# Performance work log

Measured on AMD Instinct MI355X. Metric: run time of the kernel, lower is better.

## Reference

```python
import jax, jax.numpy as jnp
import numpy as np

C = 64          # channels
K = 15          # sum(shell_sizes)=1+14
H = 32          # neighbors per query
N = 50000       # support points (== query points M)
RADIUS = 1.0
SIGMA = 0.7
INF = 1e6
BN_EPS = 1e-5


def _init_kernel_points(key):
    # stand-in for load_kernels: 1 center point + 14 points on a sphere shell
    pts = jax.random.normal(key, (K - 1, 3), dtype=jnp.float32)
    pts = pts / jnp.linalg.norm(pts, axis=1, keepdims=True) * RADIUS
    return jnp.concatenate([jnp.zeros((1, 3), jnp.float32), pts], axis=0)


def setup_inputs() -> dict:
    key = jax.random.key(0)
    ks = jax.random.split(key, 10)
    q_pts = jax.random.normal(ks[0], (N, 3), dtype=jnp.float32)
    s_pts = jax.random.normal(ks[1], (N, 3), dtype=jnp.float32)
    s_feats = jax.random.normal(ks[2], (N, C), dtype=jnp.float32)
    neighb_inds = jax.random.randint(ks[3], (N, H), 0, N)
    kernel_points = _init_kernel_points(ks[4])
    # alpha_mlp: Linear(C->C, no bias) -> BatchNorm -> LeakyReLU(0.1) -> Linear(C->K*C)
    lim1 = 1.0 / np.sqrt(C)
    W1 = jax.random.uniform(ks[5], (C, C), jnp.float32, -lim1, lim1)
    gamma = jnp.ones((C,), jnp.float32)
    beta = jnp.zeros((C,), jnp.float32)
    W2 = jax.random.uniform(ks[6], (C, K * C), jnp.float32, -lim1, lim1)
    b2 = jax.random.uniform(ks[7], (K * C,), jnp.float32, -lim1, lim1)
    return {"q_pts": q_pts, "s_pts": s_pts, "s_feats": s_feats,
            "neighb_inds": neighb_inds, "kernel_points": kernel_points,
            "W1": W1, "gamma": gamma, "beta": beta, "W2": W2, "b2": b2}


def reference(q_pts, s_pts, s_feats, neighb_inds, kernel_points, W1, gamma, beta, W2, b2):
    M = q_pts.shape[0]
    # alpha_mlp on pooled (= center) features: (M, C) -> (M, K*C)
    h = s_feats @ W1
    mu = jnp.mean(h, axis=0)
    var = jnp.var(h, axis=0)
    h = (h - mu) / jnp.sqrt(var + BN_EPS) * gamma + beta
    h = jax.nn.leaky_relu(h, 0.1)
    conv_weights = (h @ W2 + b2).reshape(M, K, C)

    # gather neighbor features with a zero padding row (index N -> zeros)
    padded_feats = jnp.concatenate([s_feats, jnp.zeros((1, C), s_feats.dtype)], axis=0)
    neighbor_feats = padded_feats[neighb_inds]                 # (M, H, C)

    # relative neighbor positions with inf padding point
    s_pts_pad = jnp.concatenate([s_pts, jnp.full((1, 3), INF, s_pts.dtype)], axis=0)
    neighbors = s_pts_pad[neighb_inds] - q_pts[:, None, :]     # (M, H, 3)

    # kernel-point influence: nearest kernel point + linear influence
    diff = neighbors[:, :, None, :] - kernel_points            # (M, H, K, 3)
    sq_d = jnp.sum(diff * diff, axis=-1)                       # (M, H, K)
    nn_sq = jnp.min(sq_d, axis=-1)                             # (M, H)
    nn_idx = jnp.argmin(sq_d, axis=-1)                         # (M, H)
    infl = jnp.clip(1.0 - jnp.sqrt(nn_sq) / SIGMA, 0.0)        # (M, H)

    # per-neighbor channel weights from the MLP output, gathered by 1nn kernel point
    nw = jnp.take_along_axis(conv_weights, nn_idx[:, :, None], axis=1)  # (M, H, C)
    nw = nw * infl[:, :, None]

    # weighted aggregation (merge=mul, aggr=sum over neighbors)
    return jnp.sum(neighbor_feats * nw, axis=1)                # (M, C)
```

## Files before the change

### kernel.cpp

```cpp
#include <hip/hip_runtime.h>
#include <math.h>

#define N_PTS 50000
#define CCH   64
#define KP    15
#define NH    32
#define SIGMA 0.7f
#define BN_EPS 1e-5f
#define LEAKY 0.1f
#define QB    16
#define CWS   18
#define STATS_BLOCKS 1024

typedef short bf16x8 __attribute__((ext_vector_type(8)));
typedef float floatx4 __attribute__((ext_vector_type(4)));

__device__ __forceinline__ unsigned short f2b(float f) {
    union { float f; unsigned u; } v; v.f = f;
    return (unsigned short)((v.u + 0x7FFFu + ((v.u >> 16) & 1u)) >> 16);
}
__device__ __forceinline__ float b2f(unsigned short b) {
    union { unsigned u; float f; } v; v.u = ((unsigned)b) << 16;
    return v.f;
}

__global__ __launch_bounds__(256) void k_prep(const float* __restrict__ sf,
                                              const float* __restrict__ W1,
                                              const float* __restrict__ W2,
                                              float* __restrict__ bn,
                                              unsigned short* __restrict__ hst,
                                              unsigned short* __restrict__ w2b,
                                              unsigned short* __restrict__ sfb) {
    int t = threadIdx.x;
    if (blockIdx.x >= STATS_BLOCKS) {
        int g = (blockIdx.x - STATS_BLOCKS) * 256 + t;
        int lane = g & 63, s = (g >> 6) & 1, tt = g >> 7;
        int col = lane & 15, quad = lane >> 4;
        int base = (s * 32 + quad * 8) * 960 + tt * 16 + col;
        ushort4 lo, hi;
        lo.x = f2b(W2[base + 0 * 960]); lo.y = f2b(W2[base + 1 * 960]);
        lo.z = f2b(W2[base + 2 * 960]); lo.w = f2b(W2[base + 3 * 960]);
        hi.x = f2b(W2[base + 4 * 960]); hi.y = f2b(W2[base + 5 * 960]);
        hi.z = f2b(W2[base + 6 * 960]); hi.w = f2b(W2[base + 7 * 960]);
        *(ushort4*)(w2b + g * 8)     = lo;
        *(ushort4*)(w2b + g * 8 + 4) = hi;
        return;
    }
    int c = t & 63, ml = t >> 6;
    float w1c[64];
    #pragma unroll
    for (int i = 0; i < 64; ++i) w1c[i] = W1[i * 64 + c];
    __shared__ float rows[4][64];
    float acc_s = 0.f, acc_q = 0.f;
    for (int m0 = blockIdx.x * 4; m0 < N_PTS; m0 += STATS_BLOCKS * 4) {
        __syncthreads();
        float v = sf[m0 * 64 + t];
        ((float*)rows)[t] = v;
        sfb[m0 * 64 + t] = f2b(v);
        __syncthreads();
        float h = 0.f;
        #pragma unroll
        for (int i4 = 0; i4 < 16; ++i4) {
            float4 r = *(const float4*)&rows[ml][i4 * 4];
            h += r.x * w1c[i4 * 4] + r.y * w1c[i4 * 4 + 1]
               + r.z * w1c[i4 * 4 + 2] + r.w * w1c[i4 * 4 + 3];
        }
        acc_s += h;
        acc_q += h * h;
        hst[(m0 + ml) * 64 + c] = f2b(h);
    }
    __shared__ float red[2][256];
    red[0][t] = acc_s; red[1][t] = acc_q;
    __syncthreads();
    if (t < 64) {
        float s = red[0][t] + red[0][64 + t] + red[0][128 + t] + red[0][192 + t];
        float q = red[1][t] + red[1][64 + t] + red[1][128 + t] + red[1][192 + t];
        atomicAdd(&bn[t], s);
        atomicAdd(&bn[64 + t], q);
    }
}

__global__ __launch_bounds__(256, 4) void k_main(
    const float* __restrict__ q_pts, const float* __restrict__ s_pts,
    const unsigned short* __restrict__ sfb, const int* __restrict__ nb,
    const float* __restrict__ kpts, const float* __restrict__ gamma,
    const float* __restrict__ beta, const float* __restrict__ bn,
    const float* __restrict__ b2, const unsigned short* __restrict__ w2b,
    const unsigned short* __restrict__ hst, float* __restrict__ out) {

    __shared__ __align__(16) unsigned short cwT[960 * CWS];
    __shared__ float abS[128];
    __shared__ int      nCnt[QB];
    __shared__ unsigned nPack[QB][NH];
    __shared__ float    nInf[QB][NH];

    int t = threadIdx.x;
    int lane = t & 63, wv = t >> 6;
    int m0 = blockIdx.x * QB;

    if (t < 64) {
        float mu  = bn[t] * (1.0f / N_PTS);
        float var = bn[64 + t] * (1.0f / N_PTS) - mu * mu;
        float a   = gamma[t] * rsqrtf(var + BN_EPS);
        abS[t]      = a;
        abS[64 + t] = beta[t] - mu * a;
    } else if (t >= 64 && t < 64 + QB) {
        nCnt[t - 64] = 0;
    }
    ((unsigned*)nPack)[t]    = 0u;
    ((unsigned*)nPack)[t + 256] = 0u;
    ((float*)nInf)[t]        = 0.f;
    ((float*)nInf)[t + 256]  = 0.f;
    __syncthreads();

    int row = lane & 15, half = lane >> 4;
    bf16x8 a0, a1;
    {
        const unsigned short* hrow = hst + (m0 + row) * 64 + half * 8;
        bf16x8 r0 = *(const bf16x8*)(hrow);
        bf16x8 r1 = *(const bf16x8*)(hrow + 32);
        #pragma unroll
        for (int j = 0; j < 8; ++j) {
            int c0 = half * 8 + j;
            float g0 = abS[c0] * b2f((unsigned short)r0[j]) + abS[64 + c0];
            g0 = g0 > 0.f ? g0 : LEAKY * g0;
            a0[j] = (short)f2b(g0);
            int c1 = 32 + c0;
            float g1 = abS[c1] * b2f((unsigned short)r1[j]) + abS[64 + c1];
            g1 = g1 > 0.f ? g1 : LEAKY * g1;
            a1[j] = (short)f2b(g1);
        }
    }

    {
        int col = lane & 15, quad = lane >> 4;
        for (int ti = 0; ti < 15; ++ti) {
            int tt = wv * 15 + ti;
            bf16x8 bf0 = *(const bf16x8*)(w2b + ((tt * 2 + 0) * 64 + lane) * 8);
            bf16x8 bf1 = *(const bf16x8*)(w2b + ((tt * 2 + 1) * 64 + lane) * 8);
            floatx4 acc = {0.f, 0.f, 0.f, 0.f};
            acc = __builtin_amdgcn_mfma_f32_16x16x32_bf16(a0, bf0, acc, 0, 0, 0);
            acc = __builtin_amdgcn_mfma_f32_16x16x32_bf16(a1, bf1, acc, 0, 0, 0);
            int n = tt * 16 + col;
            float bb = b2[n];
            unsigned short* dst = &cwT[n * CWS + quad * 4];
            ushort2 w01, w23;
            w01.x = f2b(acc[0] + bb); w01.y = f2b(acc[1] + bb);
            w23.x = f2b(acc[2] + bb); w23.y = f2b(acc[3] + bb);
            *(ushort2*)(dst)     = w01;
            *(ushort2*)(dst + 2) = w23;
        }
    }

    float kpr[45];
    #pragma unroll
    for (int i = 0; i < 45; ++i) kpr[i] = kpts[i];

    for (int task = t; task < QB * NH; task += 256) {
        int q = task >> 5, hh = task & 31;
        int m = m0 + q;
        int idx = nb[m * NH + hh];
        float px = s_pts[idx * 3 + 0] - q_pts[m * 3 + 0];
        float py = s_pts[idx * 3 + 1] - q_pts[m * 3 + 1];
        float pz = s_pts[idx * 3 + 2] - q_pts[m * 3 + 2];
        float best = 1e30f; int bi = 0;
        #pragma unroll
        for (int k = 0; k < KP; ++k) {
            float dx = px - kpr[k * 3], dy = py - kpr[k * 3 + 1], dz = pz - kpr[k * 3 + 2];
            float d = dx * dx + dy * dy + dz * dz;
            if (d < best) { best = d; bi = k; }
        }
        float infl = 1.f - sqrtf(best) * (1.0f / SIGMA);
        if (infl > 0.f) {
            int pos = atomicAdd(&nCnt[q], 1);
            nPack[q][pos] = (unsigned)idx | ((unsigned)(bi * (64 * CWS)) << 16);
            nInf[q][pos]  = infl;
        }
    }
    __syncthreads();

    {
        int c = lane;
        #pragma unroll
        for (int pp = 0; pp < 2; ++pp) {
            int qa = wv * 4 + pp * 2, qb = qa + 1;
            const unsigned short* cwa = cwT + c * CWS + qa;
            const unsigned short* cwb = cwa + 1;
            int nA = nCnt[qa], nB = nCnt[qb];
            int na = nA > nB ? nA : nB;
            float accA = 0.f, accB = 0.f;
            for (int jj = 0; jj < na; jj += 2) {
                uint2  pa = *(const uint2*)&nPack[qa][jj];
                uint2  pb = *(const uint2*)&nPack[qb][jj];
                float2 ia = *(const float2*)&nInf[qa][jj];
                float2 ib = *(const float2*)&nInf[qb][jj];
                float fA0 = b2f(sfb[(pa.x & 0xFFFFu) * 64 + c]);
                float fA1 = b2f(sfb[(pa.y & 0xFFFFu) * 64 + c]);
                float fB0 = b2f(sfb[(pb.x & 0xFFFFu) * 64 + c]);
                float fB1 = b2f(sfb[(pb.y & 0xFFFFu) * 64 + c]);
                float wA0 = b2f(cwa[pa.x >> 16]);
                float wA1 = b2f(cwa[pa.y >> 16]);
                float wB0 = b2f(cwb[pb.x >> 16]);
                float wB1 = b2f(cwb[pb.y >> 16]);
                accA += ia.x * fA0 * wA0 + ia.y * fA1 * wA1;
                accB += ib.x * fB0 * wB0 + ib.y * fB1 * wB1;
            }
            out[(m0 + qa) * 64 + c] = accA;
            out[(m0 + qb) * 64 + c] = accB;
        }
    }
}

extern "C" void kernel_launch(void* const* d_in, const int* in_sizes, int n_in,
                              void* d_out, int out_size, void* d_ws, size_t ws_size,
                              hipStream_t stream) {
    const float* q_pts   = (const float*)d_in[0];
    const float* s_pts   = (const float*)d_in[1];
    const float* s_feats = (const float*)d_in[2];
    const int*   nb      = (const int*)d_in[3];
    const float* kpts    = (const float*)d_in[4];
    const float* W1      = (const float*)d_in[5];
    const float* gamma   = (const float*)d_in[6];
    const float* beta    = (const float*)d_in[7];
    const float* W2      = (const float*)d_in[8];
    const float* b2      = (const float*)d_in[9];
    float* out = (float*)d_out;

    float* ws = (float*)d_ws;
    float* bn = ws;
    unsigned short* w2b = (unsigned short*)(ws + 128);
    unsigned short* hst = w2b + 61440;
    unsigned short* sfb = hst + N_PTS * CCH;

    hipMemsetAsync(bn, 0, 128 * sizeof(float), stream);
    k_prep<<<STATS_BLOCKS + 30, 256, 0, stream>>>(s_feats, W1, W2, bn, hst, w2b, sfb);
    k_main<<<N_PTS / QB, 256, 0, stream>>>(q_pts, s_pts, sfb, nb, kpts,
                                           gamma, beta, bn, b2, w2b, hst, out);
}
```

Before: 159.4 us.

## Repack conv weights as channel-pair words and vectorize neighbor aggregation

Each lane now handles a pair of channels for one query instead of one channel for two queries. The per-query conv weights are stored in LDS as packed bf16 pairs in a padded [k][c2][q] layout, written directly from a transposed MFMA output. The aggregation loop processes four neighbors per iteration, using 32-bit feature and weight loads and float2 output stores, which halves the number of gather and LDS load instructions. The trade-off is that the loop runs to the larger neighbor count of the two queries sharing a wave, and 4-wide steps may read padded zero entries.

```diff
diff --git a/kernel.cpp b/kernel.cpp
--- a/kernel.cpp
+++ b/kernel.cpp
@@ -9,8 +9,8 @@
 #define BN_EPS 1e-5f
 #define LEAKY 0.1f
 #define QB    16
-#define CWS   18
 #define STATS_BLOCKS 1024
+#define CW_KSTRIDE_B 2176
 
 typedef short bf16x8 __attribute__((ext_vector_type(8)));
 typedef float floatx4 __attribute__((ext_vector_type(4)));
@@ -21,6 +21,14 @@
 }
 __device__ __forceinline__ float b2f(unsigned short b) {
     union { unsigned u; float f; } v; v.u = ((unsigned)b) << 16;
+    return v.f;
+}
+__device__ __forceinline__ float blo(unsigned u) {
+    union { unsigned u; float f; } v; v.u = u << 16;
+    return v.f;
+}
+__device__ __forceinline__ float bhi(unsigned u) {
+    union { unsigned u; float f; } v; v.u = u & 0xFFFF0000u;
     return v.f;
 }
 
@@ -88,7 +96,7 @@
     const float* __restrict__ b2, const unsigned short* __restrict__ w2b,
     const unsigned short* __restrict__ hst, float* __restrict__ out) {
 
-    __shared__ __align__(16) unsigned short cwT[960 * CWS];
+    __shared__ __align__(16) unsigned cwP[KP * 32 * 17];
     __shared__ float abS[128];
     __shared__ int      nCnt[QB];
     __shared__ unsigned nPack[QB][NH];
@@ -107,10 +115,10 @@
     } else if (t >= 64 && t < 64 + QB) {
         nCnt[t - 64] = 0;
     }
-    ((unsigned*)nPack)[t]    = 0u;
+    ((unsigned*)nPack)[t]       = 0u;
     ((unsigned*)nPack)[t + 256] = 0u;
-    ((float*)nInf)[t]        = 0.f;
-    ((float*)nInf)[t + 256]  = 0.f;
+    ((float*)nInf)[t]           = 0.f;
+    ((float*)nInf)[t + 256]     = 0.f;
     __syncthreads();
 
     int row = lane & 15, half = lane >> 4;
@@ -133,22 +141,24 @@
     }
 
     {
-        int col = lane & 15, quad = lane >> 4;
+        int q = lane & 15, quad = lane >> 4;
+        #pragma unroll 3
         for (int ti = 0; ti < 15; ++ti) {
             int tt = wv * 15 + ti;
             bf16x8 bf0 = *(const bf16x8*)(w2b + ((tt * 2 + 0) * 64 + lane) * 8);
             bf16x8 bf1 = *(const bf16x8*)(w2b + ((tt * 2 + 1) * 64 + lane) * 8);
             floatx4 acc = {0.f, 0.f, 0.f, 0.f};
-            acc = __builtin_amdgcn_mfma_f32_16x16x32_bf16(a0, bf0, acc, 0, 0, 0);
-            acc = __builtin_amdgcn_mfma_f32_16x16x32_bf16(a1, bf1, acc, 0, 0, 0);
-            int n = tt * 16 + col;
-            float bb = b2[n];
-            unsigned short* dst = &cwT[n * CWS + quad * 4];
-            ushort2 w01, w23;
-            w01.x = f2b(acc[0] + bb); w01.y = f2b(acc[1] + bb);
-            w23.x = f2b(acc[2] + bb); w23.y = f2b(acc[3] + bb);
-            *(ushort2*)(dst)     = w01;
-            *(ushort2*)(dst + 2) = w23;
+            acc = __builtin_amdgcn_mfma_f32_16x16x32_bf16(bf0, a0, acc, 0, 0, 0);
+            acc = __builtin_amdgcn_mfma_f32_16x16x32_bf16(bf1, a1, acc, 0, 0, 0);
+            int n0 = tt * 16 + quad * 4;
+            float4 bb = *(const float4*)&b2[n0];
+            int k  = n0 >> 6;
+            int c2 = (n0 & 63) >> 1;
+            unsigned w0 = (unsigned)f2b(acc[0] + bb.x) | ((unsigned)f2b(acc[1] + bb.y) << 16);
+            unsigned w1 = (unsigned)f2b(acc[2] + bb.z) | ((unsigned)f2b(acc[3] + bb.w) << 16);
+            unsigned* dst = cwP + (k * 544 + c2 * 17 + q);
+            dst[0]  = w0;
+            dst[17] = w1;
         }
     }
 
@@ -173,40 +183,48 @@
         float infl = 1.f - sqrtf(best) * (1.0f / SIGMA);
         if (infl > 0.f) {
             int pos = atomicAdd(&nCnt[q], 1);
-            nPack[q][pos] = (unsigned)idx | ((unsigned)(bi * (64 * CWS)) << 16);
+            nPack[q][pos] = (unsigned)idx | ((unsigned)(bi * CW_KSTRIDE_B) << 16);
             nInf[q][pos]  = infl;
         }
     }
     __syncthreads();
 
     {
-        int c = lane;
+        int r = lane >> 5, c2 = lane & 31;
+        const unsigned short* sfbC = sfb + c2 * 2;
+        const unsigned char* cwB = (const unsigned char*)cwP;
         #pragma unroll
         for (int pp = 0; pp < 2; ++pp) {
-            int qa = wv * 4 + pp * 2, qb = qa + 1;
-            const unsigned short* cwa = cwT + c * CWS + qa;
-            const unsigned short* cwb = cwa + 1;
-            int nA = nCnt[qa], nB = nCnt[qb];
+            int qa = wv * 4 + pp * 2;
+            int q  = qa + r;
+            const unsigned* packRow = &nPack[q][0];
+            const float*    infRow  = &nInf[q][0];
+            const unsigned char* cwLane = cwB + (c2 * 17 + q) * 4;
+            int nA = nCnt[qa], nB = nCnt[qa + 1];
             int na = nA > nB ? nA : nB;
-            float accA = 0.f, accB = 0.f;
-            for (int jj = 0; jj < na; jj += 2) {
-                uint2  pa = *(const uint2*)&nPack[qa][jj];
-                uint2  pb = *(const uint2*)&nPack[qb][jj];
-                float2 ia = *(const float2*)&nInf[qa][jj];
-                float2 ib = *(const float2*)&nInf[qb][jj];
-                float fA0 = b2f(sfb[(pa.x & 0xFFFFu) * 64 + c]);
-                float fA1 = b2f(sfb[(pa.y & 0xFFFFu) * 64 + c]);
-                float fB0 = b2f(sfb[(pb.x & 0xFFFFu) * 64 + c]);
-                float fB1 = b2f(sfb[(pb.y & 0xFFFFu) * 64 + c]);
-                float wA0 = b2f(cwa[pa.x >> 16]);
-                float wA1 = b2f(cwa[pa.y >> 16]);
-                float wB0 = b2f(cwb[pb.x >> 16]);
-                float wB1 = b2f(cwb[pb.y >> 16]);
-                accA += ia.x * fA0 * wA0 + ia.y * fA1 * wA1;
-                accB += ib.x * fB0 * wB0 + ib.y * fB1 * wB1;
+            float acc0 = 0.f, acc1 = 0.f;
+            for (int jj = 0; jj < na; jj += 4) {
+                uint4  pk = *(const uint4*)&packRow[jj];
+                float4 in = *(const float4*)&infRow[jj];
+                unsigned f0 = *(const unsigned*)(sfbC + (pk.x & 0xFFFFu) * 64);
+                unsigned f1 = *(const unsigned*)(sfbC + (pk.y & 0xFFFFu) * 64);
+                unsigned f2 = *(const unsigned*)(sfbC + (pk.z & 0xFFFFu) * 64);
+                unsigned f3 = *(const unsigned*)(sfbC + (pk.w & 0xFFFFu) * 64);
+                unsigned w0 = *(const unsigned*)(cwLane + (pk.x >> 16));
+                unsigned w1 = *(const unsigned*)(cwLane + (pk.y >> 16));
+                unsigned w2 = *(const unsigned*)(cwLane + (pk.z >> 16));
+                unsigned w3 = *(const unsigned*)(cwLane + (pk.w >> 16));
+                acc0 = fmaf(in.x * blo(f0), blo(w0), acc0);
+                acc1 = fmaf(in.x * bhi(f0), bhi(w0), acc1);
+                acc0 = fmaf(in.y * blo(f1), blo(w1), acc0);
+                acc1 = fmaf(in.y * bhi(f1), bhi(w1), acc1);
+                acc0 = fmaf(in.z * blo(f2), blo(w2), acc0);
+                acc1 = fmaf(in.z * bhi(f2), bhi(w2), acc1);
+                acc0 = fmaf(in.w * blo(f3), blo(w3), acc0);
+                acc1 = fmaf(in.w * bhi(f3), bhi(w3), acc1);
             }
-            out[(m0 + qa) * 64 + c] = accA;
-            out[(m0 + qb) * 64 + c] = accB;
+            float2 o; o.x = acc0; o.y = acc1;
+            *(float2*)&out[(m0 + q) * 64 + c2 * 2] = o;
         }
     }
 }
```

New measurement: 159.3 us. About the same (-0.1%).
